# Optimization experiments

Measured on AMD Instinct MI355X. Metric: run time of the kernel, lower is better.

## Reference

```python
import jax, jax.numpy as jnp
import numpy as np


def setup_inputs() -> dict:
    key = jax.random.key(0)
    k1, k2, k3, k4 = jax.random.split(key, 4)
    H = W = 1024
    B = 8
    image = jax.random.uniform(k1, (1, H, W), dtype=jnp.float32)
    x = jax.random.normal(k2, (B, 1, H, W), dtype=jnp.float32)
    KL_w = jax.random.normal(k3, (9, 1, 3, 3), dtype=jnp.float32) * 0.3
    KL_b = jax.random.normal(k4, (9,), dtype=jnp.float32) * 0.1
    return {"image": image, "x": x, "KL_w": KL_w, "KL_b": KL_b}


def reference(image, x, KL_w, KL_b):
    # Per-pixel 3x3 kernel prediction: Conv2d(1, 9, k=3, padding='same')
    # image: (1, H, W) -> add batch dim -> (1, 1, H, W)
    K = jax.lax.conv_general_dilated(
        image[None], KL_w, window_strides=(1, 1), padding='SAME',
        dimension_numbers=('NCHW', 'OIHW', 'NCHW'))[0]  # (9, H, W)
    K = K + KL_b[:, None, None]

    H, W = x.shape[-2], x.shape[-1]
    xpad = jnp.pad(x, ((0, 0), (0, 0), (1, 1), (1, 1)))  # (B, C, H+2, W+2)

    # y[b,c,h,w] = sum_{a,d} xpad[b,c,h+a,w+d] * K[3a+d,h,w]
    y = jnp.zeros_like(x)
    for a in range(3):
        for d in range(3):
            y = y + xpad[..., a:a + H, d:d + W] * K[3 * a + d]
    return y
```

## Files before the change

kernel.cpp:

```cpp
#include <hip/hip_runtime.h>


#define H  1024
#define W  1024
#define NB 8
#define TD 32
#define TP 34
#define TT (TP * TP)

__global__ __launch_bounds__(256)
void smblock_kernel(const float* __restrict__ image,
                    const float* __restrict__ x,
                    const float* __restrict__ kw,
                    const float* __restrict__ kb,
                    float* __restrict__ y)
{
    __shared__ float simg[TT];
    __shared__ float sx[2][TT];

    const int h0  = blockIdx.y * TD;
    const int w0  = blockIdx.x * TD;
    const int tid = threadIdx.x;

    #pragma unroll
    for (int k = 0; k < 5; ++k) {
        int idx = tid + k * 256;
        if (idx < TT) {
            int rr = idx / TP, cc = idx - rr * TP;
            int h = h0 + rr - 1, w = w0 + cc - 1;
            bool ok = ((unsigned)h < H) && ((unsigned)w < W);
            size_t g = (size_t)h * W + w;
            simg[idx]  = ok ? image[g] : 0.f;
            sx[0][idx] = ok ? x[g]     : 0.f;
        }
    }
    __syncthreads();

    const int c  = tid & 31;
    const int r0 = tid >> 5;

    float K[4][9];
    #pragma unroll
    for (int p = 0; p < 4; ++p) {
        #pragma unroll
        for (int j = 0; j < 9; ++j) K[p][j] = kb[j];
        int r = r0 + p * 8;
        #pragma unroll
        for (int a = 0; a < 3; ++a) {
            #pragma unroll
            for (int d = 0; d < 3; ++d) {
                float iv = simg[(r + a) * TP + (c + d)];
                #pragma unroll
                for (int j = 0; j < 9; ++j)
                    K[p][j] += kw[j * 9 + a * 3 + d] * iv;
            }
        }
    }

    #pragma unroll
    for (int b = 0; b < NB; ++b) {
        const float* sxb = sx[b & 1];

        float pre[5];
        if (b + 1 < NB) {
            const float* xn = x + (size_t)(b + 1) * (H * W);
            #pragma unroll
            for (int k = 0; k < 5; ++k) {
                int idx = tid + k * 256;
                float v = 0.f;
                if (idx < TT) {
                    int rr = idx / TP, cc = idx - rr * TP;
                    int h = h0 + rr - 1, w = w0 + cc - 1;
                    if (((unsigned)h < H) && ((unsigned)w < W))
                        v = xn[(size_t)h * W + w];
                }
                pre[k] = v;
            }
        }

        #pragma unroll
        for (int p = 0; p < 4; ++p) {
            int r = r0 + p * 8;
            float acc = 0.f;
            #pragma unroll
            for (int a = 0; a < 3; ++a)
                #pragma unroll
                for (int d = 0; d < 3; ++d)
                    acc += sxb[(r + a) * TP + (c + d)] * K[p][3 * a + d];
            y[((size_t)b * H + (h0 + r)) * W + (w0 + c)] = acc;
        }

        if (b + 1 < NB) {
            float* dst = sx[(b + 1) & 1];
            #pragma unroll
            for (int k = 0; k < 5; ++k) {
                int idx = tid + k * 256;
                if (idx < TT) dst[idx] = pre[k];
            }
            __syncthreads();
        }
    }
}

extern "C" void kernel_launch(void* const* d_in, const int* in_sizes, int n_in,
                              void* d_out, int out_size, void* d_ws, size_t ws_size,
                              hipStream_t stream)
{
    const float* image = (const float*)d_in[0];
    const float* x     = (const float*)d_in[1];
    const float* kw    = (const float*)d_in[2];
    const float* kb    = (const float*)d_in[3];
    float* y = (float*)d_out;

    dim3 grid(W / TD, H / TD);
    smblock_kernel<<<grid, 256, 0, stream>>>(image, x, kw, kb, y);
}
```

Baseline: 102.5 us.

## Vectorize tile loads and stores with float4 and 4-wide per-thread column blocking

Each thread now owns four adjacent columns of one row instead of four rows of one column. Interior tile loads, prefetches and output stores use float4, and halo cells are loaded by dedicated lanes in each wavefront. The shared memory row stride is padded to 36 floats so that float4/float2 LDS reads are aligned and neighbouring columns are reused across the 3x3 window. This is meant to cut the number of global and LDS transactions and the index arithmetic, at the cost of a more complex halo assignment and some possible LDS bank conflicts.

```diff
diff --git a/kernel.cpp b/kernel.cpp
--- a/kernel.cpp
+++ b/kernel.cpp
@@ -6,7 +6,8 @@
 #define NB 8
 #define TD 32
 #define TP 34
-#define TT (TP * TP)
+#define LS 36
+#define LT (TP * LS)
 
 __global__ __launch_bounds__(256)
 void smblock_kernel(const float* __restrict__ image,
@@ -15,88 +16,99 @@
                     const float* __restrict__ kb,
                     float* __restrict__ y)
 {
-    __shared__ float simg[TT];
-    __shared__ float sx[2][TT];
+    __shared__ float simg[LT];
+    __shared__ float sx[2][LT];
 
     const int h0  = blockIdx.y * TD;
     const int w0  = blockIdx.x * TD;
     const int tid = threadIdx.x;
+    const int r   = tid >> 3;
+    const int cg  = tid & 7;
 
-    #pragma unroll
-    for (int k = 0; k < 5; ++k) {
-        int idx = tid + k * 256;
-        if (idx < TT) {
-            int rr = idx / TP, cc = idx - rr * TP;
-            int h = h0 + rr - 1, w = w0 + cc - 1;
-            bool ok = ((unsigned)h < H) && ((unsigned)w < W);
-            size_t g = (size_t)h * W + w;
-            simg[idx]  = ok ? image[g] : 0.f;
-            sx[0][idx] = ok ? x[g]     : 0.f;
-        }
+    const size_t gint = (size_t)(h0 + r) * W + (w0 + 4 * cg);
+    const int    lint = (r + 1) * LS + (4 * cg + 1);
+
+    int hr = -1, hc = -1;
+    {
+        const int wv = tid >> 6, ln = tid & 63;
+        if      (wv == 0) { if (ln < TP) { hr = 0;      hc = ln;     } }
+        else if (wv == 1) { if (ln < TP) { hr = TP - 1; hc = ln;     } }
+        else if (wv == 2) { if (ln < TD) { hr = ln + 1; hc = 0;      } }
+        else              { if (ln < TD) { hr = ln + 1; hc = TP - 1; } }
+    }
+    const bool has_halo = (hr >= 0);
+    const int  gh = h0 + hr - 1, gw = w0 + hc - 1;
+    const bool hin = has_halo && ((unsigned)gh < H) && ((unsigned)gw < W);
+    const size_t ghalo = (size_t)gh * W + gw;
+    const int    lhalo = hr * LS + hc;
+
+    {
+        float4 iv = *(const float4*)(image + gint);
+        float4 xv = *(const float4*)(x + gint);
+        float ihv = hin ? image[ghalo] : 0.f;
+        float xhv = hin ? x[ghalo]     : 0.f;
+        simg[lint]  = iv.x; simg[lint+1]  = iv.y; simg[lint+2]  = iv.z; simg[lint+3]  = iv.w;
+        sx[0][lint] = xv.x; sx[0][lint+1] = xv.y; sx[0][lint+2] = xv.z; sx[0][lint+3] = xv.w;
+        if (has_halo) { simg[lhalo] = ihv; sx[0][lhalo] = xhv; }
     }
     __syncthreads();
 
-    const int c  = tid & 31;
-    const int r0 = tid >> 5;
-
     float K[4][9];
     #pragma unroll
-    for (int p = 0; p < 4; ++p) {
+    for (int j = 0; j < 4; ++j)
         #pragma unroll
-        for (int j = 0; j < 9; ++j) K[p][j] = kb[j];
-        int r = r0 + p * 8;
+        for (int t = 0; t < 9; ++t) K[j][t] = kb[t];
+
+    #pragma unroll
+    for (int a = 0; a < 3; ++a) {
+        const float* row = &simg[(r + a) * LS + 4 * cg];
+        float4 f4 = *(const float4*)row;
+        float2 f2 = *(const float2*)(row + 4);
+        float wv[6] = { f4.x, f4.y, f4.z, f4.w, f2.x, f2.y };
         #pragma unroll
-        for (int a = 0; a < 3; ++a) {
+        for (int d = 0; d < 3; ++d)
             #pragma unroll
-            for (int d = 0; d < 3; ++d) {
-                float iv = simg[(r + a) * TP + (c + d)];
+            for (int t = 0; t < 9; ++t) {
+                float wgt = kw[t * 9 + 3 * a + d];
                 #pragma unroll
-                for (int j = 0; j < 9; ++j)
-                    K[p][j] += kw[j * 9 + a * 3 + d] * iv;
+                for (int j = 0; j < 4; ++j)
+                    K[j][t] += wgt * wv[j + d];
             }
-        }
     }
 
     #pragma unroll
     for (int b = 0; b < NB; ++b) {
-        const float* sxb = sx[b & 1];
+        float4 pv; float phv = 0.f;
+        if (b + 1 < NB) {
+            const float* xn = x + (size_t)(b + 1) * ((size_t)H * W);
+            pv  = *(const float4*)(xn + gint);
+            if (hin) phv = xn[ghalo];
+        }
 
-        float pre[5];
-        if (b + 1 < NB) {
-            const float* xn = x + (size_t)(b + 1) * (H * W);
+        const float* sb = sx[b & 1];
+        float a0 = 0.f, a1 = 0.f, a2 = 0.f, a3 = 0.f;
+        #pragma unroll
+        for (int a = 0; a < 3; ++a) {
+            const float* row = &sb[(r + a) * LS + 4 * cg];
+            float4 f4 = *(const float4*)row;
+            float2 f2 = *(const float2*)(row + 4);
+            float wv[6] = { f4.x, f4.y, f4.z, f4.w, f2.x, f2.y };
             #pragma unroll
-            for (int k = 0; k < 5; ++k) {
-                int idx = tid + k * 256;
-                float v = 0.f;
-                if (idx < TT) {
-                    int rr = idx / TP, cc = idx - rr * TP;
-                    int h = h0 + rr - 1, w = w0 + cc - 1;
-                    if (((unsigned)h < H) && ((unsigned)w < W))
-                        v = xn[(size_t)h * W + w];
-                }
-                pre[k] = v;
+            for (int d = 0; d < 3; ++d) {
+                a0 += wv[0 + d] * K[0][3 * a + d];
+                a1 += wv[1 + d] * K[1][3 * a + d];
+                a2 += wv[2 + d] * K[2][3 * a + d];
+                a3 += wv[3 + d] * K[3][3 * a + d];
             }
         }
-
-        #pragma unroll
-        for (int p = 0; p < 4; ++p) {
-            int r = r0 + p * 8;
-            float acc = 0.f;
-            #pragma unroll
-            for (int a = 0; a < 3; ++a)
-                #pragma unroll
-                for (int d = 0; d < 3; ++d)
-                    acc += sxb[(r + a) * TP + (c + d)] * K[p][3 * a + d];
-            y[((size_t)b * H + (h0 + r)) * W + (w0 + c)] = acc;
-        }
+        float4 o; o.x = a0; o.y = a1; o.z = a2; o.w = a3;
+        *(float4*)(y + (size_t)b * ((size_t)H * W) + gint) = o;
 
         if (b + 1 < NB) {
             float* dst = sx[(b + 1) & 1];
-            #pragma unroll
-            for (int k = 0; k < 5; ++k) {
-                int idx = tid + k * 256;
-                if (idx < TT) dst[idx] = pre[k];
-            }
+            dst[lint]   = pv.x; dst[lint+1] = pv.y;
+            dst[lint+2] = pv.z; dst[lint+3] = pv.w;
+            if (has_halo) dst[lhalo] = phv;
             __syncthreads();
         }
     }
```

Result: no change. 100.9 us (-1.5%).

## Replace shared-memory tiling with register-based float4 loads per thread

Applied to the files above, without the earlier changes.

The kernel drops the LDS halo tiles and barriers. Each thread now handles four adjacent pixels, loading three float4 rows plus left and right halo scalars straight from global memory into registers. The next batch is prefetched into registers while the current one is computed, and output is written as float4. This removes LDS traffic and __syncthreads at the cost of redundant halo loads that go through cache, plus higher register pressure.

```diff
diff --git a/kernel.cpp b/kernel.cpp
--- a/kernel.cpp
+++ b/kernel.cpp
@@ -4,9 +4,7 @@
 #define H  1024
 #define W  1024
 #define NB 8
-#define TD 32
-#define TP 34
-#define TT (TP * TP)
+#define HW ((size_t)H * (size_t)W)
 
 __global__ __launch_bounds__(256)
 void smblock_kernel(const float* __restrict__ image,
@@ -15,90 +13,99 @@
                     const float* __restrict__ kb,
                     float* __restrict__ y)
 {
-    __shared__ float simg[TT];
-    __shared__ float sx[2][TT];
+    const int tid = threadIdx.x;
+    const int r   = tid >> 3;
+    const int cg  = tid & 7;
+    const int h   = (int)blockIdx.y * 32 + r;
+    const int w   = (int)blockIdx.x * 32 + 4 * cg;
 
-    const int h0  = blockIdx.y * TD;
-    const int w0  = blockIdx.x * TD;
-    const int tid = threadIdx.x;
-
-    #pragma unroll
-    for (int k = 0; k < 5; ++k) {
-        int idx = tid + k * 256;
-        if (idx < TT) {
-            int rr = idx / TP, cc = idx - rr * TP;
-            int h = h0 + rr - 1, w = w0 + cc - 1;
-            bool ok = ((unsigned)h < H) && ((unsigned)w < W);
-            size_t g = (size_t)h * W + w;
-            simg[idx]  = ok ? image[g] : 0.f;
-            sx[0][idx] = ok ? x[g]     : 0.f;
+    unsigned o4[3], ol[3], orr[3];
+    float mc[3], mlm[3], mrm[3];
+    {
+        const bool lv = (w >= 1);
+        const bool rv = (w + 4 < W);
+        #pragma unroll
+        for (int a = 0; a < 3; ++a) {
+            int hh = h + a - 1;
+            int hc = hh < 0 ? 0 : (hh > H - 1 ? H - 1 : hh);
+            unsigned ro = (unsigned)hc * W;
+            o4[a]  = ro + w;
+            ol[a]  = ro + (lv ? (w - 1) : w);
+            orr[a] = ro + (rv ? (w + 4) : w);
+            float hv = ((unsigned)hh < (unsigned)H) ? 1.f : 0.f;
+            mc[a]  = hv;
+            mlm[a] = lv ? hv : 0.f;
+            mrm[a] = rv ? hv : 0.f;
         }
     }
-    __syncthreads();
 
-    const int c  = tid & 31;
-    const int r0 = tid >> 5;
+    float nxt[18];
+    #pragma unroll
+    for (int a = 0; a < 3; ++a) {
+        float4 f = *(const float4*)(x + o4[a]);
+        nxt[6*a+0] = x[ol[a]];
+        nxt[6*a+1] = f.x; nxt[6*a+2] = f.y; nxt[6*a+3] = f.z; nxt[6*a+4] = f.w;
+        nxt[6*a+5] = x[orr[a]];
+    }
 
     float K[4][9];
     #pragma unroll
-    for (int p = 0; p < 4; ++p) {
+    for (int t = 0; t < 9; ++t) {
+        float bt = kb[t];
         #pragma unroll
-        for (int j = 0; j < 9; ++j) K[p][j] = kb[j];
-        int r = r0 + p * 8;
+        for (int j = 0; j < 4; ++j) K[j][t] = bt;
+    }
+    #pragma unroll
+    for (int a = 0; a < 3; ++a) {
+        float4 f = *(const float4*)(image + o4[a]);
+        float vl = image[ol[a]] * mlm[a];
+        float vr = image[orr[a]] * mrm[a];
+        float v[6] = { vl, f.x*mc[a], f.y*mc[a], f.z*mc[a], f.w*mc[a], vr };
+        #pragma unroll
+        for (int d = 0; d < 3; ++d)
+            #pragma unroll
+            for (int t = 0; t < 9; ++t) {
+                float wgt = kw[t * 9 + 3 * a + d];
+                #pragma unroll
+                for (int j = 0; j < 4; ++j)
+                    K[j][t] += wgt * v[j + d];
+            }
+    }
+
+    float cur[18];
+    #pragma unroll 1
+    for (int b = 0; b < NB; ++b) {
         #pragma unroll
         for (int a = 0; a < 3; ++a) {
+            cur[6*a+0] = nxt[6*a+0] * mlm[a];
+            cur[6*a+1] = nxt[6*a+1] * mc[a];
+            cur[6*a+2] = nxt[6*a+2] * mc[a];
+            cur[6*a+3] = nxt[6*a+3] * mc[a];
+            cur[6*a+4] = nxt[6*a+4] * mc[a];
+            cur[6*a+5] = nxt[6*a+5] * mrm[a];
+        }
+        if (b + 1 < NB) {
+            const float* xb = x + (size_t)(b + 1) * HW;
+            #pragma unroll
+            for (int a = 0; a < 3; ++a) {
+                float4 f = *(const float4*)(xb + o4[a]);
+                nxt[6*a+0] = xb[ol[a]];
+                nxt[6*a+1] = f.x; nxt[6*a+2] = f.y; nxt[6*a+3] = f.z; nxt[6*a+4] = f.w;
+                nxt[6*a+5] = xb[orr[a]];
+            }
+        }
+        float a0 = 0.f, a1 = 0.f, a2 = 0.f, a3 = 0.f;
+        #pragma unroll
+        for (int a = 0; a < 3; ++a)
             #pragma unroll
             for (int d = 0; d < 3; ++d) {
-                float iv = simg[(r + a) * TP + (c + d)];
-                #pragma unroll
-                for (int j = 0; j < 9; ++j)
-                    K[p][j] += kw[j * 9 + a * 3 + d] * iv;
+                a0 += cur[6*a + 0 + d] * K[0][3*a+d];
+                a1 += cur[6*a + 1 + d] * K[1][3*a+d];
+                a2 += cur[6*a + 2 + d] * K[2][3*a+d];
+                a3 += cur[6*a + 3 + d] * K[3][3*a+d];
             }
-        }
-    }
-
-    #pragma unroll
-    for (int b = 0; b < NB; ++b) {
-        const float* sxb = sx[b & 1];
-
-        float pre[5];
-        if (b + 1 < NB) {
-            const float* xn = x + (size_t)(b + 1) * (H * W);
-            #pragma unroll
-            for (int k = 0; k < 5; ++k) {
-                int idx = tid + k * 256;
-                float v = 0.f;
-                if (idx < TT) {
-                    int rr = idx / TP, cc = idx - rr * TP;
-                    int h = h0 + rr - 1, w = w0 + cc - 1;
-                    if (((unsigned)h < H) && ((unsigned)w < W))
-                        v = xn[(size_t)h * W + w];
-                }
-                pre[k] = v;
-            }
-        }
-
-        #pragma unroll
-        for (int p = 0; p < 4; ++p) {
-            int r = r0 + p * 8;
-            float acc = 0.f;
-            #pragma unroll
-            for (int a = 0; a < 3; ++a)
-                #pragma unroll
-                for (int d = 0; d < 3; ++d)
-                    acc += sxb[(r + a) * TP + (c + d)] * K[p][3 * a + d];
-            y[((size_t)b * H + (h0 + r)) * W + (w0 + c)] = acc;
-        }
-
-        if (b + 1 < NB) {
-            float* dst = sx[(b + 1) & 1];
-            #pragma unroll
-            for (int k = 0; k < 5; ++k) {
-                int idx = tid + k * 256;
-                if (idx < TT) dst[idx] = pre[k];
-            }
-            __syncthreads();
-        }
+        float4 o; o.x = a0; o.y = a1; o.z = a2; o.w = a3;
+        *(float4*)(y + (size_t)b * HW + (size_t)((unsigned)h * W + w)) = o;
     }
 }
 
@@ -112,6 +119,6 @@
     const float* kb    = (const float*)d_in[3];
     float* y = (float*)d_out;
 
-    dim3 grid(W / TD, H / TD);
+    dim3 grid(W / 32, H / 32);
     smblock_kernel<<<grid, 256, 0, stream>>>(image, x, kw, kb, y);
 }
```

After: 102.6 us. About the same (+0.1%).
